# Optimization experiments

Hardware: AMD Instinct MI355X
Metric: run time of the kernel (lower is better)

Reference implementation:

```python
import jax, jax.numpy as jnp
import numpy as np
import math

T_MIN = 0.1
T_MAX = 1.0


def setup_inputs() -> dict:
    key = jax.random.key(0)
    k1, k2, k3, k4, k5, k6 = jax.random.split(key, 6)
    B, H, SQ, SK, DK = 1, 16, 4096, 4096, 64
    query = jax.random.normal(k1, (B, H, SQ, DK), dtype=jnp.float32)
    key_t = jax.random.normal(k2, (B, H, SK, DK), dtype=jnp.float32)
    # MLP params (3 -> 16 -> 1). Original zero-inits the last layer; we use
    # small random values so gradients flow to query/key in the bwd test.
    W1 = jax.random.normal(k3, (16, 3), dtype=jnp.float32) * 0.5
    b1 = jax.random.normal(k4, (16,), dtype=jnp.float32) * 0.1
    W2 = jax.random.normal(k5, (1, 16), dtype=jnp.float32) * 0.5
    b2 = jax.random.normal(k6, (1,), dtype=jnp.float32) * 0.1
    return {"query": query, "key": key_t, "W1": W1, "b1": b1, "W2": W2, "b2": b2}


def reference(query, key, W1, b1, W2, b2):
    d_k = query.shape[-1]
    sk = key.shape[-2]
    q = query.astype(jnp.float32)
    k = key.astype(jnp.float32)
    # [B,H,Sq,Sk] score matrix
    scores = jnp.einsum('bhqd,bhkd->bhqk', q, k) / math.sqrt(d_k)
    scores = jnp.clip(scores, -50.0, 50.0)
    mean_sim = scores.mean(axis=(-2, -1))                 # [B,H]
    max_sim = scores.max(axis=-1).mean(axis=-1)           # [B,H]
    probs = jax.nn.softmax(scores / 2.0, axis=-1)         # [B,H,Sq,Sk]
    # torch .var(dim=-1) is unbiased (divisor Sk-1)
    pm = probs.mean(axis=-1, keepdims=True)
    var = ((probs - pm) ** 2).sum(axis=-1) / (sk - 1)     # [B,H,Sq]
    entropy_proxy = var.mean(axis=-1)                     # [B,H]
    mean_sim = jnp.clip(mean_sim, -10.0, 10.0)
    max_sim = jnp.clip(max_sim, -10.0, 10.0)
    entropy_proxy = jnp.clip(entropy_proxy, 0.0, 1.0)
    features = jnp.stack([mean_sim, max_sim, entropy_proxy], axis=-1)  # [B,H,3]
    h = jnp.tanh(features @ W1.T + b1)
    raw_t = h @ W2.T + b2                                 # [B,H,1]
    t = T_MIN + jax.nn.sigmoid(raw_t) * (T_MAX - T_MIN)
    t = jnp.clip(t, T_MIN, T_MAX)
    return t[..., None].astype(query.dtype)               # [B,H,1,1]
```

## Files before the change

### kernel.cpp

```cpp
#include <hip/hip_runtime.h>
#include <math.h>

#define NH   16
#define SQL  4096
#define SKL  4096
#define DK   64
#define QB   128
#define KB   64
#define KSPLIT 2
#define KHALF (SKL / KSPLIT)
#define NKT   (KHALF / KB)

#define QSCALE  0.090168440f
#define UNSCALE 1.3862943611f

#define NB2      (NH * 32 * KSPLIT)
#define ROWFLOAT (NB2 * QB)
#define STATS_BYTES ((size_t)(NB2 + 3 * ROWFLOAT) * 4)

#define KIMG 8192
#define QIMG 16384
#define KPRE_BYTES ((size_t)NH * 64 * KIMG)
#define QPRE_BYTES ((size_t)NH * 32 * QIMG)

typedef __bf16 bf16x8 __attribute__((ext_vector_type(8)));
typedef __bf16 bf16x4 __attribute__((ext_vector_type(4)));
typedef float  f32x4  __attribute__((ext_vector_type(4)));
typedef float  f32x2  __attribute__((ext_vector_type(2)));

#if __has_builtin(__builtin_amdgcn_exp2f)
#define EXP2(x) __builtin_amdgcn_exp2f(x)
#else
#define EXP2(x) exp2f(x)
#endif

static __device__ __forceinline__ f32x2 pk_fma(f32x2 a, f32x2 b, f32x2 c) {
#if __has_builtin(__builtin_elementwise_fma)
    return __builtin_elementwise_fma(a, b, c);
#else
    f32x2 r; r[0] = fmaf(a[0], b[0], c[0]); r[1] = fmaf(a[1], b[1], c[1]); return r;
#endif
}
static __device__ __forceinline__ f32x2 pk_max(f32x2 a, f32x2 b) {
#if __has_builtin(__builtin_elementwise_max)
    return __builtin_elementwise_max(a, b);
#else
    f32x2 r; r[0] = fmaxf(a[0], b[0]); r[1] = fmaxf(a[1], b[1]); return r;
#endif
}

__device__ __forceinline__ int swz(int row, int col_bytes) {
    return ((row << 7) + col_bytes) ^ ((row & 7) << 4);
}

static __device__ __forceinline__ void gld16(void* l, const void* g) {
#if __has_builtin(__builtin_amdgcn_global_load_lds)
    __builtin_amdgcn_global_load_lds(
        (const __attribute__((address_space(1))) unsigned int*)g,
        (__attribute__((address_space(3))) unsigned int*)l,
        16, 0, 0);
#else
    *reinterpret_cast<float4*>(l) = *reinterpret_cast<const float4*>(g);
#endif
}

__global__ __launch_bounds__(512) void dtp_prepack(const float* __restrict__ Q,
                                                   const float* __restrict__ K,
                                                   unsigned char* __restrict__ Qpre,
                                                   unsigned char* __restrict__ Kpre) {
    const int i   = blockIdx.x * 512 + threadIdx.x;
    const int c16 = i & 7;
    const int rg  = i >> 3;
    const int h   = rg >> 12;
    const int row = rg & 4095;

    const float* ks = K + (size_t)rg * DK + c16 * 8;
    float4 a = *reinterpret_cast<const float4*>(ks);
    float4 b = *reinterpret_cast<const float4*>(ks + 4);
    bf16x8 kv;
    kv[0]=(__bf16)a.x; kv[1]=(__bf16)a.y; kv[2]=(__bf16)a.z; kv[3]=(__bf16)a.w;
    kv[4]=(__bf16)b.x; kv[5]=(__bf16)b.y; kv[6]=(__bf16)b.z; kv[7]=(__bf16)b.w;
    *reinterpret_cast<bf16x8*>(
        &Kpre[(size_t)h * 64 * KIMG + (size_t)(row >> 6) * KIMG + swz(row & 63, c16 * 16)]) = kv;

    const float* qs = Q + (size_t)rg * DK + c16 * 8;
    float4 c = *reinterpret_cast<const float4*>(qs);
    float4 d = *reinterpret_cast<const float4*>(qs + 4);
    bf16x8 qv;
    qv[0]=(__bf16)(c.x*QSCALE); qv[1]=(__bf16)(c.y*QSCALE);
    qv[2]=(__bf16)(c.z*QSCALE); qv[3]=(__bf16)(c.w*QSCALE);
    qv[4]=(__bf16)(d.x*QSCALE); qv[5]=(__bf16)(d.y*QSCALE);
    qv[6]=(__bf16)(d.z*QSCALE); qv[7]=(__bf16)(d.w*QSCALE);
    *reinterpret_cast<bf16x8*>(
        &Qpre[(size_t)h * 32 * QIMG + (size_t)(row >> 7) * QIMG + swz(row & 127, c16 * 16)]) = qv;
}

__global__ __launch_bounds__(256, 4) void dtp_stats_glds(const unsigned char* __restrict__ Qpre,
                                                         const unsigned char* __restrict__ Kpre,
                                                         float* __restrict__ RSUM,
                                                         float* __restrict__ RMX,
                                                         float* __restrict__ RS1,
                                                         float* __restrict__ RS2) {
    __shared__ __align__(16) unsigned char Qs[QIMG];
    __shared__ __align__(16) unsigned char Ks[2][KIMG];
    __shared__ float red[32];

    const int qb   = blockIdx.x;
    const int h    = blockIdx.y;
    const int half = blockIdx.z;
    const int tid  = threadIdx.x;
    const int lane = tid & 63;
    const int w    = tid >> 6;
    const int l15  = lane & 15;
    const int lg   = lane >> 4;

    const unsigned char* Qg = Qpre + (size_t)(h * 32 + qb) * QIMG;
    const unsigned char* Kg = Kpre + (size_t)h * 64 * KIMG + (size_t)half * NKT * KIMG;

    {
        const int off = tid * 16;
        #pragma unroll
        for (int r2 = 0; r2 < 4; ++r2)
            gld16(&Qs[off + r2 * 4096], Qg + off + r2 * 4096);
        gld16(&Ks[0][off],        Kg + off);
        gld16(&Ks[0][off + 4096], Kg + off + 4096);
    }
    __syncthreads();

    bf16x8 aF[2][2];
    #pragma unroll
    for (int rt = 0; rt < 2; ++rt) {
        int r = w * 32 + rt * 16 + l15;
        aF[rt][0] = *reinterpret_cast<const bf16x8*>(&Qs[swz(r, 0 * 64 + lg * 16)]);
        aF[rt][1] = *reinterpret_cast<const bf16x8*>(&Qs[swz(r, 1 * 64 + lg * 16)]);
    }

    f32x2 rsum[2][2], rmx[2][2], rs1[2][2], rs2[2][2];
    #pragma unroll
    for (int rt = 0; rt < 2; ++rt)
        #pragma unroll
        for (int p = 0; p < 2; ++p) {
            rsum[rt][p] = (f32x2){0.f, 0.f};
            rmx[rt][p]  = (f32x2){-3.0e38f, -3.0e38f};
            rs1[rt][p]  = (f32x2){0.f, 0.f};
            rs2[rt][p]  = (f32x2){0.f, 0.f};
        }

    for (int t = 0; t < NKT; ++t) {
        const int b = t & 1;

        if (t + 1 < NKT) {
            const unsigned char* Kt = Kg + (size_t)(t + 1) * KIMG;
            const int off = tid * 16;
            gld16(&Ks[b ^ 1][off],        Kt + off);
            gld16(&Ks[b ^ 1][off + 4096], Kt + off + 4096);
        }

        #pragma unroll
        for (int ct = 0; ct < 4; ++ct) {
            int rr = ct * 16 + l15;
            bf16x8 b0 = *reinterpret_cast<const bf16x8*>(&Ks[b][swz(rr, 0 * 64 + lg * 16)]);
            bf16x8 b1 = *reinterpret_cast<const bf16x8*>(&Ks[b][swz(rr, 1 * 64 + lg * 16)]);
            #pragma unroll
            for (int rt = 0; rt < 2; ++rt) {
                f32x4 a = {0.f, 0.f, 0.f, 0.f};
                a = __builtin_amdgcn_mfma_f32_16x16x32_bf16(aF[rt][0], b0, a, 0, 0, 0);
                a = __builtin_amdgcn_mfma_f32_16x16x32_bf16(aF[rt][1], b1, a, 0, 0, 0);
                f32x2 v01 = __builtin_shufflevector(a, a, 0, 1);
                f32x2 v23 = __builtin_shufflevector(a, a, 2, 3);
                rsum[rt][0] += v01; rsum[rt][1] += v23;
                rmx[rt][0] = pk_max(rmx[rt][0], v01);
                rmx[rt][1] = pk_max(rmx[rt][1], v23);
                f32x2 e01, e23;
                e01[0] = EXP2(v01[0]); e01[1] = EXP2(v01[1]);
                e23[0] = EXP2(v23[0]); e23[1] = EXP2(v23[1]);
                rs1[rt][0] += e01; rs1[rt][1] += e23;
                rs2[rt][0] = pk_fma(e01, e01, rs2[rt][0]);
                rs2[rt][1] = pk_fma(e23, e23, rs2[rt][1]);
            }
        }

        __syncthreads();
    }

    #pragma unroll
    for (int m = 1; m < 16; m <<= 1) {
        #pragma unroll
        for (int rt = 0; rt < 2; ++rt)
            #pragma unroll
            for (int c = 0; c < 2; ++c) {
                rsum[rt][c][0] += __shfl_xor(rsum[rt][c][0], m, 64);
                rsum[rt][c][1] += __shfl_xor(rsum[rt][c][1], m, 64);
                rmx[rt][c][0]   = fmaxf(rmx[rt][c][0], __shfl_xor(rmx[rt][c][0], m, 64));
                rmx[rt][c][1]   = fmaxf(rmx[rt][c][1], __shfl_xor(rmx[rt][c][1], m, 64));
                rs1[rt][c][0]  += __shfl_xor(rs1[rt][c][0], m, 64);
                rs1[rt][c][1]  += __shfl_xor(rs1[rt][c][1], m, 64);
                rs2[rt][c][0]  += __shfl_xor(rs2[rt][c][0], m, 64);
                rs2[rt][c][1]  += __shfl_xor(rs2[rt][c][1], m, 64);
            }
    }

    const int base = (h * 32 + qb) * KSPLIT + half;
    if (l15 == 0) {
        float bs = 0.f;
        #pragma unroll
        for (int rt = 0; rt < 2; ++rt) {
            const size_t rb = (size_t)base * QB + (w * 32 + rt * 16 + lg * 4);
            float4 mx = {rmx[rt][0][0] * UNSCALE, rmx[rt][0][1] * UNSCALE,
                         rmx[rt][1][0] * UNSCALE, rmx[rt][1][1] * UNSCALE};
            float4 s1 = {rs1[rt][0][0], rs1[rt][0][1], rs1[rt][1][0], rs1[rt][1][1]};
            float4 s2 = {rs2[rt][0][0], rs2[rt][0][1], rs2[rt][1][0], rs2[rt][1][1]};
            *reinterpret_cast<float4*>(&RMX[rb]) = mx;
            *reinterpret_cast<float4*>(&RS1[rb]) = s1;
            *reinterpret_cast<float4*>(&RS2[rb]) = s2;
            bs += (rsum[rt][0][0] + rsum[rt][0][1]) + (rsum[rt][1][0] + rsum[rt][1][1]);
        }
        red[w * 8 + lg * 2 + 0] = bs;
        red[w * 8 + lg * 2 + 1] = 0.f;
    }
    __syncthreads();
    if (tid == 0) {
        float bs = 0.f;
        #pragma unroll
        for (int i = 0; i < 32; ++i) bs += red[i];
        RSUM[base] = bs * UNSCALE;
    }
}

__global__ __launch_bounds__(512, 8) void dtp_stats_reg(const float* __restrict__ Q,
                                                        const float* __restrict__ K,
                                                        float* __restrict__ RSUM,
                                                        float* __restrict__ RMX,
                                                        float* __restrict__ RS1,
                                                        float* __restrict__ RS2) {
    __shared__ __align__(16) unsigned char Qs[QB * DK * 2];
    __shared__ __align__(16) unsigned char Ks[2][KB * DK * 2];
    __shared__ float red[32];

    const int qb = blockIdx.x, h = blockIdx.y, half = blockIdx.z;
    const int tid = threadIdx.x, lane = tid & 63, w = tid >> 6;
    const int l15 = lane & 15, lg = lane >> 4;

    const float* Qh = Q + ((size_t)h * SQL + (size_t)qb * QB) * DK;
    const float* Kh = K + ((size_t)h * SKL + (size_t)half * KHALF) * DK;
    const int sc4 = tid & 15, sr = tid >> 4;

    #pragma unroll
    for (int j = 0; j < 4; ++j) {
        int r = sr + 32 * j;
        const float4 v = *reinterpret_cast<const float4*>(Qh + r * DK + sc4 * 4);
        bf16x4 hv;
        hv[0] = (__bf16)(v.x * QSCALE); hv[1] = (__bf16)(v.y * QSCALE);
        hv[2] = (__bf16)(v.z * QSCALE); hv[3] = (__bf16)(v.w * QSCALE);
        *reinterpret_cast<bf16x4*>(&Qs[swz(r, sc4 * 8)]) = hv;
    }
    float4 kreg[2];
    #pragma unroll
    for (int j = 0; j < 2; ++j)
        kreg[j] = *reinterpret_cast<const float4*>(Kh + (size_t)(sr + 32 * j) * DK + sc4 * 4);
    #pragma unroll
    for (int j = 0; j < 2; ++j) {
        int r = sr + 32 * j;
        bf16x4 hv;
        hv[0] = (__bf16)kreg[j].x; hv[1] = (__bf16)kreg[j].y;
        hv[2] = (__bf16)kreg[j].z; hv[3] = (__bf16)kreg[j].w;
        *reinterpret_cast<bf16x4*>(&Ks[0][swz(r, sc4 * 8)]) = hv;
    }
    #pragma unroll
    for (int j = 0; j < 2; ++j)
        kreg[j] = *reinterpret_cast<const float4*>(Kh + (size_t)(KB + sr + 32 * j) * DK + sc4 * 4);
    __syncthreads();

    bf16x8 aF[2];
    {
        int r = w * 16 + l15;
        aF[0] = *reinterpret_cast<const bf16x8*>(&Qs[swz(r, 0 * 64 + lg * 16)]);
        aF[1] = *reinterpret_cast<const bf16x8*>(&Qs[swz(r, 1 * 64 + lg * 16)]);
    }
    f32x2 rsum01 = {0.f,0.f}, rsum23 = {0.f,0.f};
    f32x2 rmx01 = {-3.0e38f,-3.0e38f}, rmx23 = {-3.0e38f,-3.0e38f};
    f32x2 rs1_01 = {0.f,0.f}, rs1_23 = {0.f,0.f};
    f32x2 rs2_01 = {0.f,0.f}, rs2_23 = {0.f,0.f};

    for (int kt = 0; kt < NKT; ++kt) {
        const int cur = kt & 1;
        if (kt + 1 < NKT) {
            #pragma unroll
            for (int j = 0; j < 2; ++j) {
                int r = sr + 32 * j;
                bf16x4 hv;
                hv[0] = (__bf16)kreg[j].x; hv[1] = (__bf16)kreg[j].y;
                hv[2] = (__bf16)kreg[j].z; hv[3] = (__bf16)kreg[j].w;
                *reinterpret_cast<bf16x4*>(&Ks[cur ^ 1][swz(r, sc4 * 8)]) = hv;
            }
            if (kt + 2 < NKT) {
                const float* Kt = Kh + (size_t)(kt + 2) * KB * DK;
                #pragma unroll
                for (int j = 0; j < 2; ++j)
                    kreg[j] = *reinterpret_cast<const float4*>(Kt + (size_t)(sr + 32 * j) * DK + sc4 * 4);
            }
        }
        #pragma unroll
        for (int ct = 0; ct < 4; ++ct) {
            int rr = ct * 16 + l15;
            bf16x8 b0 = *reinterpret_cast<const bf16x8*>(&Ks[cur][swz(rr, 0 * 64 + lg * 16)]);
            bf16x8 b1 = *reinterpret_cast<const bf16x8*>(&Ks[cur][swz(rr, 1 * 64 + lg * 16)]);
            f32x4 a = {0.f, 0.f, 0.f, 0.f};
            a = __builtin_amdgcn_mfma_f32_16x16x32_bf16(aF[0], b0, a, 0, 0, 0);
            a = __builtin_amdgcn_mfma_f32_16x16x32_bf16(aF[1], b1, a, 0, 0, 0);
            f32x2 v01 = __builtin_shufflevector(a, a, 0, 1);
            f32x2 v23 = __builtin_shufflevector(a, a, 2, 3);
            rsum01 += v01; rsum23 += v23;
            rmx01 = pk_max(rmx01, v01); rmx23 = pk_max(rmx23, v23);
            f32x2 e01, e23;
            e01[0] = EXP2(v01[0]); e01[1] = EXP2(v01[1]);
            e23[0] = EXP2(v23[0]); e23[1] = EXP2(v23[1]);
            rs1_01 += e01; rs1_23 += e23;
            rs2_01 = pk_fma(e01, e01, rs2_01);
            rs2_23 = pk_fma(e23, e23, rs2_23);
        }
        __syncthreads();
    }
    #pragma unroll
    for (int m = 1; m < 16; m <<= 1) {
        #pragma unroll
        for (int c = 0; c < 2; ++c) {
            rsum01[c] += __shfl_xor(rsum01[c], m, 64);
            rsum23[c] += __shfl_xor(rsum23[c], m, 64);
            rmx01[c] = fmaxf(rmx01[c], __shfl_xor(rmx01[c], m, 64));
            rmx23[c] = fmaxf(rmx23[c], __shfl_xor(rmx23[c], m, 64));
            rs1_01[c] += __shfl_xor(rs1_01[c], m, 64);
            rs1_23[c] += __shfl_xor(rs1_23[c], m, 64);
            rs2_01[c] += __shfl_xor(rs2_01[c], m, 64);
            rs2_23[c] += __shfl_xor(rs2_23[c], m, 64);
        }
    }
    const int base = (h * 32 + qb) * KSPLIT + half;
    if (l15 == 0) {
        const size_t rb = (size_t)base * QB + (w * 16 + lg * 4);
        float4 mx = {rmx01[0]*UNSCALE, rmx01[1]*UNSCALE, rmx23[0]*UNSCALE, rmx23[1]*UNSCALE};
        float4 s1 = {rs1_01[0], rs1_01[1], rs1_23[0], rs1_23[1]};
        float4 s2 = {rs2_01[0], rs2_01[1], rs2_23[0], rs2_23[1]};
        *reinterpret_cast<float4*>(&RMX[rb]) = mx;
        *reinterpret_cast<float4*>(&RS1[rb]) = s1;
        *reinterpret_cast<float4*>(&RS2[rb]) = s2;
        red[w * 4 + lg] = (rsum01[0] + rsum01[1]) + (rsum23[0] + rsum23[1]);
    }
    __syncthreads();
    if (tid == 0) {
        float bs = 0.f;
        #pragma unroll
        for (int i = 0; i < 32; ++i) bs += red[i];
        RSUM[base] = bs * UNSCALE;
    }
}

__global__ __launch_bounds__(256) void dtp_finalize(const float* __restrict__ RSUM,
                                                    const float* __restrict__ RMX,
                                                    const float* __restrict__ RS1,
                                                    const float* __restrict__ RS2,
                                                    const float* __restrict__ W1,
                                                    const float* __restrict__ b1,
                                                    const float* __restrict__ W2,
                                                    const float* __restrict__ b2,
                                                    float* __restrict__ out) {
    const int h   = blockIdx.x;
    const int tid = threadIdx.x;
    const float invSK  = 1.0f / (float)SKL;
    const float invSK1 = 1.0f / (float)(SKL - 1);

    float sm = 0.f, sv = 0.f;
    #pragma unroll
    for (int j = 0; j < 16; ++j) {
        int r  = tid + 256 * j;
        int qb = r >> 7;
        int rr = r & 127;
        size_t b0  = ((size_t)(h * 32 + qb) * KSPLIT) * QB + rr;
        size_t b1i = b0 + QB;
        float mx = fmaxf(RMX[b0], RMX[b1i]);
        float s1 = RS1[b0] + RS1[b1i];
        float s2 = RS2[b0] + RS2[b1i];
        sm += mx;
        sv += (s2 / (s1 * s1) - invSK) * invSK1;
    }
    float ss = (tid < 64) ? RSUM[h * 64 + (tid & 63)] : 0.f;
    #pragma unroll
    for (int m = 1; m < 64; m <<= 1) {
        sm += __shfl_xor(sm, m, 64);
        sv += __shfl_xor(sv, m, 64);
        ss += __shfl_xor(ss, m, 64);
    }
    __shared__ float redm[4], redv[4], reds[4];
    const int wv = tid >> 6;
    if ((tid & 63) == 0) { redm[wv] = sm; redv[wv] = sv; reds[wv] = ss; }
    __syncthreads();
    if (tid == 0) {
        float tsm = redm[0] + redm[1] + redm[2] + redm[3];
        float tsv = redv[0] + redv[1] + redv[2] + redv[3];
        float tss = reds[0];
        float mean_sim = tss / ((float)SQL * (float)SKL);
        float max_sim  = tsm / (float)SQL;
        float entropy  = tsv / (float)SQL;
        mean_sim = fminf(fmaxf(mean_sim, -10.f), 10.f);
        max_sim  = fminf(fmaxf(max_sim,  -10.f), 10.f);
        entropy  = fminf(fmaxf(entropy,    0.f), 1.f);
        float raw = b2[0];
        #pragma unroll
        for (int i = 0; i < 16; ++i) {
            float a = b1[i] + W1[i*3+0] * mean_sim + W1[i*3+1] * max_sim + W1[i*3+2] * entropy;
            raw += W2[i] * tanhf(a);
        }
        float t = 0.1f + 0.9f / (1.0f + __expf(-raw));
        t = fminf(fmaxf(t, 0.1f), 1.0f);
        out[h] = t;
    }
}

extern "C" void kernel_launch(void* const* d_in, const int* in_sizes, int n_in,
                              void* d_out, int out_size, void* d_ws, size_t ws_size,
                              hipStream_t stream) {
    const float* Q  = (const float*)d_in[0];
    const float* K  = (const float*)d_in[1];
    const float* W1 = (const float*)d_in[2];
    const float* b1 = (const float*)d_in[3];
    const float* W2 = (const float*)d_in[4];
    const float* b2 = (const float*)d_in[5];
    float* out      = (float*)d_out;

    float* RSUM = (float*)d_ws;
    float* RMX  = RSUM + NB2;
    float* RS1  = RMX + ROWFLOAT;
    float* RS2  = RS1 + ROWFLOAT;

    const size_t need = STATS_BYTES + QPRE_BYTES + KPRE_BYTES;
    dim3 grid(SQL / QB, NH, KSPLIT);

    if (ws_size >= need) {
        unsigned char* Qpre = (unsigned char*)d_ws + STATS_BYTES;
        unsigned char* Kpre = Qpre + QPRE_BYTES;
        dtp_prepack<<<1024, 512, 0, stream>>>(Q, K, Qpre, Kpre);
        dtp_stats_glds<<<grid, 256, 0, stream>>>(Qpre, Kpre, RSUM, RMX, RS1, RS2);
    } else {
        dtp_stats_reg<<<grid, 512, 0, stream>>>(Q, K, RSUM, RMX, RS1, RS2);
    }
    dtp_finalize<<<NH, 256, 0, stream>>>(RSUM, RMX, RS1, RS2, W1, b1, W2, b2, out);
}
```

Before: 76.93 us.

## Retile stats kernel warps as 2x2 grid over query rows and key columns

Each of the four warps now covers 64 query rows and 32 key columns, where before it covered 32 rows and all 64 key columns of each tile. This halves the K-fragment LDS reads per warp per tile and raises the number of independent MFMA chains. In exchange each warp holds twice as many Q fragments and accumulators in registers, and a shared-memory cross-warp reduction is added to combine the two column halves before the per-row stats are stored.

```diff
diff --git a/kernel.cpp b/kernel.cpp
--- a/kernel.cpp
+++ b/kernel.cpp
@@ -103,7 +103,10 @@
                                                          float* __restrict__ RS2) {
     __shared__ __align__(16) unsigned char Qs[QIMG];
     __shared__ __align__(16) unsigned char Ks[2][KIMG];
-    __shared__ float red[32];
+    __shared__ float redS1[2][QB];
+    __shared__ float redS2[2][QB];
+    __shared__ float redMX[2][QB];
+    __shared__ float redR[16];
 
     const int qb   = blockIdx.x;
     const int h    = blockIdx.y;
@@ -111,73 +114,93 @@
     const int tid  = threadIdx.x;
     const int lane = tid & 63;
     const int w    = tid >> 6;
+    const int rh   = w >> 1;
+    const int ch   = w & 1;
     const int l15  = lane & 15;
     const int lg   = lane >> 4;
 
     const unsigned char* Qg = Qpre + (size_t)(h * 32 + qb) * QIMG;
     const unsigned char* Kg = Kpre + (size_t)h * 64 * KIMG + (size_t)half * NKT * KIMG;
-
-    {
-        const int off = tid * 16;
-        #pragma unroll
-        for (int r2 = 0; r2 < 4; ++r2)
-            gld16(&Qs[off + r2 * 4096], Qg + off + r2 * 4096);
-        gld16(&Ks[0][off],        Kg + off);
-        gld16(&Ks[0][off + 4096], Kg + off + 4096);
-    }
+    const int off = tid * 16;
+
+    #pragma unroll
+    for (int r2 = 0; r2 < 4; ++r2)
+        gld16(&Qs[off + r2 * 4096], Qg + off + r2 * 4096);
+    gld16(&Ks[0][off],        Kg + off);
+    gld16(&Ks[0][off + 4096], Kg + off + 4096);
     __syncthreads();
 
-    bf16x8 aF[2][2];
-    #pragma unroll
-    for (int rt = 0; rt < 2; ++rt) {
-        int r = w * 32 + rt * 16 + l15;
+    bf16x8 aF[4][2];
+    #pragma unroll
+    for (int rt = 0; rt < 4; ++rt) {
+        int r = rh * 64 + rt * 16 + l15;
         aF[rt][0] = *reinterpret_cast<const bf16x8*>(&Qs[swz(r, 0 * 64 + lg * 16)]);
         aF[rt][1] = *reinterpret_cast<const bf16x8*>(&Qs[swz(r, 1 * 64 + lg * 16)]);
     }
 
-    f32x2 rsum[2][2], rmx[2][2], rs1[2][2], rs2[2][2];
-    #pragma unroll
-    for (int rt = 0; rt < 2; ++rt)
+    f32x2 rsum[4][2], rs1[4][2], rs2[4][2];
+    float rmx[4][4];
+    #pragma unroll
+    for (int rt = 0; rt < 4; ++rt) {
         #pragma unroll
         for (int p = 0; p < 2; ++p) {
             rsum[rt][p] = (f32x2){0.f, 0.f};
-            rmx[rt][p]  = (f32x2){-3.0e38f, -3.0e38f};
             rs1[rt][p]  = (f32x2){0.f, 0.f};
             rs2[rt][p]  = (f32x2){0.f, 0.f};
         }
+        #pragma unroll
+        for (int r = 0; r < 4; ++r) rmx[rt][r] = -3.0e38f;
+    }
 
     for (int t = 0; t < NKT; ++t) {
         const int b = t & 1;
 
         if (t + 1 < NKT) {
             const unsigned char* Kt = Kg + (size_t)(t + 1) * KIMG;
-            const int off = tid * 16;
             gld16(&Ks[b ^ 1][off],        Kt + off);
             gld16(&Ks[b ^ 1][off + 4096], Kt + off + 4096);
         }
 
-        #pragma unroll
-        for (int ct = 0; ct < 4; ++ct) {
-            int rr = ct * 16 + l15;
-            bf16x8 b0 = *reinterpret_cast<const bf16x8*>(&Ks[b][swz(rr, 0 * 64 + lg * 16)]);
-            bf16x8 b1 = *reinterpret_cast<const bf16x8*>(&Ks[b][swz(rr, 1 * 64 + lg * 16)]);
-            #pragma unroll
-            for (int rt = 0; rt < 2; ++rt) {
-                f32x4 a = {0.f, 0.f, 0.f, 0.f};
-                a = __builtin_amdgcn_mfma_f32_16x16x32_bf16(aF[rt][0], b0, a, 0, 0, 0);
-                a = __builtin_amdgcn_mfma_f32_16x16x32_bf16(aF[rt][1], b1, a, 0, 0, 0);
-                f32x2 v01 = __builtin_shufflevector(a, a, 0, 1);
-                f32x2 v23 = __builtin_shufflevector(a, a, 2, 3);
-                rsum[rt][0] += v01; rsum[rt][1] += v23;
-                rmx[rt][0] = pk_max(rmx[rt][0], v01);
-                rmx[rt][1] = pk_max(rmx[rt][1], v23);
-                f32x2 e01, e23;
-                e01[0] = EXP2(v01[0]); e01[1] = EXP2(v01[1]);
-                e23[0] = EXP2(v23[0]); e23[1] = EXP2(v23[1]);
-                rs1[rt][0] += e01; rs1[rt][1] += e23;
-                rs2[rt][0] = pk_fma(e01, e01, rs2[rt][0]);
-                rs2[rt][1] = pk_fma(e23, e23, rs2[rt][1]);
-            }
+        bf16x8 bF[2][2];
+        #pragma unroll
+        for (int ct = 0; ct < 2; ++ct) {
+            int rr = ch * 32 + ct * 16 + l15;
+            bF[ct][0] = *reinterpret_cast<const bf16x8*>(&Ks[b][swz(rr, 0 * 64 + lg * 16)]);
+            bF[ct][1] = *reinterpret_cast<const bf16x8*>(&Ks[b][swz(rr, 1 * 64 + lg * 16)]);
+        }
+
+        #pragma unroll
+        for (int rt = 0; rt < 4; ++rt) {
+            f32x4 a0 = {0.f, 0.f, 0.f, 0.f};
+            a0 = __builtin_amdgcn_mfma_f32_16x16x32_bf16(aF[rt][0], bF[0][0], a0, 0, 0, 0);
+            a0 = __builtin_amdgcn_mfma_f32_16x16x32_bf16(aF[rt][1], bF[0][1], a0, 0, 0, 0);
+            f32x4 a1 = {0.f, 0.f, 0.f, 0.f};
+            a1 = __builtin_amdgcn_mfma_f32_16x16x32_bf16(aF[rt][0], bF[1][0], a1, 0, 0, 0);
+            a1 = __builtin_amdgcn_mfma_f32_16x16x32_bf16(aF[rt][1], bF[1][1], a1, 0, 0, 0);
+
+            f32x2 p0 = __builtin_shufflevector(a0, a0, 0, 1);
+            f32x2 q0 = __builtin_shufflevector(a0, a0, 2, 3);
+            f32x2 p1 = __builtin_shufflevector(a1, a1, 0, 1);
+            f32x2 q1 = __builtin_shufflevector(a1, a1, 2, 3);
+
+            rsum[rt][0] += p0 + p1;
+            rsum[rt][1] += q0 + q1;
+
+            rmx[rt][0] = fmaxf(fmaxf(a0[0], a1[0]), rmx[rt][0]);
+            rmx[rt][1] = fmaxf(fmaxf(a0[1], a1[1]), rmx[rt][1]);
+            rmx[rt][2] = fmaxf(fmaxf(a0[2], a1[2]), rmx[rt][2]);
+            rmx[rt][3] = fmaxf(fmaxf(a0[3], a1[3]), rmx[rt][3]);
+
+            f32x2 e0, e1, f0, f1;
+            e0[0] = EXP2(p0[0]); e0[1] = EXP2(p0[1]);
+            f0[0] = EXP2(q0[0]); f0[1] = EXP2(q0[1]);
+            e1[0] = EXP2(p1[0]); e1[1] = EXP2(p1[1]);
+            f1[0] = EXP2(q1[0]); f1[1] = EXP2(q1[1]);
+
+            rs1[rt][0] += e0 + e1;
+            rs1[rt][1] += f0 + f1;
+            rs2[rt][0] = pk_fma(e0, e0, pk_fma(e1, e1, rs2[rt][0]));
+            rs2[rt][1] = pk_fma(f0, f0, pk_fma(f1, f1, rs2[rt][1]));
         }
 
         __syncthreads();
@@ -186,43 +209,51 @@
     #pragma unroll
     for (int m = 1; m < 16; m <<= 1) {
         #pragma unroll
-        for (int rt = 0; rt < 2; ++rt)
+        for (int rt = 0; rt < 4; ++rt) {
             #pragma unroll
             for (int c = 0; c < 2; ++c) {
                 rsum[rt][c][0] += __shfl_xor(rsum[rt][c][0], m, 64);
                 rsum[rt][c][1] += __shfl_xor(rsum[rt][c][1], m, 64);
-                rmx[rt][c][0]   = fmaxf(rmx[rt][c][0], __shfl_xor(rmx[rt][c][0], m, 64));
-                rmx[rt][c][1]   = fmaxf(rmx[rt][c][1], __shfl_xor(rmx[rt][c][1], m, 64));
                 rs1[rt][c][0]  += __shfl_xor(rs1[rt][c][0], m, 64);
                 rs1[rt][c][1]  += __shfl_xor(rs1[rt][c][1], m, 64);
                 rs2[rt][c][0]  += __shfl_xor(rs2[rt][c][0], m, 64);
                 rs2[rt][c][1]  += __shfl_xor(rs2[rt][c][1], m, 64);
             }
-    }
-
-    const int base = (h * 32 + qb) * KSPLIT + half;
+            #pragma unroll
+            for (int r = 0; r < 4; ++r)
+                rmx[rt][r] = fmaxf(rmx[rt][r], __shfl_xor(rmx[rt][r], m, 64));
+        }
+    }
+
     if (l15 == 0) {
         float bs = 0.f;
         #pragma unroll
-        for (int rt = 0; rt < 2; ++rt) {
-            const size_t rb = (size_t)base * QB + (w * 32 + rt * 16 + lg * 4);
-            float4 mx = {rmx[rt][0][0] * UNSCALE, rmx[rt][0][1] * UNSCALE,
-                         rmx[rt][1][0] * UNSCALE, rmx[rt][1][1] * UNSCALE};
-            float4 s1 = {rs1[rt][0][0], rs1[rt][0][1], rs1[rt][1][0], rs1[rt][1][1]};
-            float4 s2 = {rs2[rt][0][0], rs2[rt][0][1], rs2[rt][1][0], rs2[rt][1][1]};
-            *reinterpret_cast<float4*>(&RMX[rb]) = mx;
-            *reinterpret_cast<float4*>(&RS1[rb]) = s1;
-            *reinterpret_cast<float4*>(&RS2[rb]) = s2;
+        for (int rt = 0; rt < 4; ++rt) {
+            int row = rh * 64 + rt * 16 + lg * 4;
+            redS1[ch][row + 0] = rs1[rt][0][0]; redS1[ch][row + 1] = rs1[rt][0][1];
+            redS1[ch][row + 2] = rs1[rt][1][0]; redS1[ch][row + 3] = rs1[rt][1][1];
+            redS2[ch][row + 0] = rs2[rt][0][0]; redS2[ch][row + 1] = rs2[rt][0][1];
+            redS2[ch][row + 2] = rs2[rt][1][0]; redS2[ch][row + 3] = rs2[rt][1][1];
+            redMX[ch][row + 0] = rmx[rt][0];    redMX[ch][row + 1] = rmx[rt][1];
+            redMX[ch][row + 2] = rmx[rt][2];    redMX[ch][row + 3] = rmx[rt][3];
             bs += (rsum[rt][0][0] + rsum[rt][0][1]) + (rsum[rt][1][0] + rsum[rt][1][1]);
         }
-        red[w * 8 + lg * 2 + 0] = bs;
-        red[w * 8 + lg * 2 + 1] = 0.f;
+        redR[w * 4 + lg] = bs;
     }
     __syncthreads();
+
+    const int base = (h * 32 + qb) * KSPLIT + half;
+    if (tid < QB) {
+        const int row = tid;
+        const size_t rb = (size_t)base * QB + row;
+        RS1[rb] = redS1[0][row] + redS1[1][row];
+        RS2[rb] = redS2[0][row] + redS2[1][row];
+        RMX[rb] = fmaxf(redMX[0][row], redMX[1][row]) * UNSCALE;
+    }
     if (tid == 0) {
         float bs = 0.f;
         #pragma unroll
-        for (int i = 0; i < 32; ++i) bs += red[i];
+        for (int i = 0; i < 16; ++i) bs += redR[i];
         RSUM[base] = bs * UNSCALE;
     }
 }
```

Result: slower. 96.54 us (+25.5%).
